# Optimization experiments

Measured on AMD Instinct MI355X. Metric: run time of the kernel, lower is better.

The kernel has to match this reference:

```python
import jax, jax.numpy as jnp
import numpy as np


def setup_inputs() -> dict:
    key = jax.random.key(0)
    k1, k2 = jax.random.split(key)
    B, S, D = 32, 1024, 384
    MAX_MEL_LEN = 8192  # >= max possible sum of durations (7*1024)
    x = jax.random.normal(k1, (B, S, D), dtype=jnp.float32)
    duration = jax.random.randint(k2, (B, S), 0, 8, dtype=jnp.int32)
    return {"x": x, "duration": duration, "max_mel_len": MAX_MEL_LEN}


def reference(x, duration, max_mel_len):
    # x: (B, S, D) float, duration: (B, S) int, max_mel_len: python int
    B, S, D = x.shape
    csum = jnp.cumsum(duration, axis=1)          # (B, S) inclusive cumsum
    mel_len = csum[:, -1]                        # (B,) expanded length per sample
    t = jnp.arange(max_mel_len, dtype=csum.dtype)  # (T,) output frame indices
    # frame t maps to token i where csum[i-1] <= t < csum[i]; side='right'
    # correctly skips zero-duration tokens (repeated csum values)
    idx = jax.vmap(lambda c: jnp.searchsorted(c, t, side='right'))(csum)  # (B, T)
    idx = jnp.clip(idx, 0, S - 1)
    out = jnp.take_along_axis(x, idx[:, :, None], axis=1)  # (B, T, D) gather
    mask = t[None, :] < mel_len[:, None]                   # (B, T) pad mask
    out = out * mask[:, :, None].astype(x.dtype)
    return out, mel_len.astype(jnp.int64)
```

## Files before the change

kernel.cpp:

```cpp
#include <hip/hip_runtime.h>


#define BATCH 32
#define SRC_S 1024
#define DIM   384
#define ROWS  32
#define C4    (DIM / 4)

__global__ void lr_cumsum_kernel(const int* __restrict__ duration,
                                 int* __restrict__ csum,
                                 float* __restrict__ mel_out) {
    __shared__ int s[SRC_S];
    const int b = blockIdx.x;
    const int tid = threadIdx.x;
    s[tid] = duration[b * SRC_S + tid];
    for (int off = 1; off < SRC_S; off <<= 1) {
        __syncthreads();
        const int add = (tid >= off) ? s[tid - off] : 0;
        __syncthreads();
        s[tid] += add;
    }
    __syncthreads();
    csum[b * SRC_S + tid] = s[tid];
    if (tid == SRC_S - 1) {
        mel_out[b] = (float)s[SRC_S - 1];
    }
}

__global__ void lr_gather_kernel(const float* __restrict__ x,
                                 const int* __restrict__ csum,
                                 float* __restrict__ out, int T) {
    __shared__ int c[SRC_S];
    __shared__ int src[ROWS];
    const int b = blockIdx.y;
    const int t0 = blockIdx.x * ROWS;
    const int tid = threadIdx.x;

    ((int4*)c)[tid] = ((const int4*)(csum + b * SRC_S))[tid];
    __syncthreads();

    const int mel_len = c[SRC_S - 1];
    if (tid < ROWS) {
        const int t = t0 + tid;
        int lo = 0, hi = SRC_S;
        while (lo < hi) {
            const int mid = (lo + hi) >> 1;
            if (c[mid] <= t) lo = mid + 1; else hi = mid;
        }
        const int idx = (lo < SRC_S - 1) ? lo : (SRC_S - 1);
        src[tid] = (t < mel_len && t < T) ? idx : ((t < T) ? -1 : -2);
    }
    __syncthreads();

    float4* __restrict__ out4 = (float4*)(out + ((size_t)b * T + t0) * DIM);
    const float4* __restrict__ x4 = (const float4*)(x + (size_t)b * SRC_S * DIM);

    #pragma unroll
    for (int i = tid; i < ROWS * C4; i += 256) {
        const int row = i / C4;
        const int col = i - row * C4;
        const int sidx = src[row];
        if (sidx == -2) continue;
        float4 v = make_float4(0.f, 0.f, 0.f, 0.f);
        if (sidx >= 0) v = x4[(size_t)sidx * C4 + col];
        out4[(size_t)row * C4 + col] = v;
    }
}

extern "C" void kernel_launch(void* const* d_in, const int* in_sizes, int n_in,
                              void* d_out, int out_size, void* d_ws, size_t ws_size,
                              hipStream_t stream) {
    const float* x = (const float*)d_in[0];
    const int* duration = (const int*)d_in[1];
    const int T = (out_size - BATCH) / (BATCH * DIM);

    int* csum = (int*)d_ws;
    float* out = (float*)d_out;
    float* mel_out = out + (size_t)BATCH * T * DIM;

    lr_cumsum_kernel<<<BATCH, SRC_S, 0, stream>>>(duration, csum, mel_out);

    dim3 grid((T + ROWS - 1) / ROWS, BATCH);
    lr_gather_kernel<<<grid, 256, 0, stream>>>(x, csum, out, T);
}
```

Measured before the change: 453.2 us.

## Precompute per-frame source index in scan kernel, drop binary search in gather

The scan kernel now scatters each token's index directly into a per-frame index array (and -1 for padded frames), replacing the csum output. The gather kernel no longer loads csum into shared memory or binary-searches; it reads the precomputed index per row, uses a fixed-trip unrolled loop, and writes output with nontemporal stores. This removes per-block shared loads, syncs and search, at the cost of a larger workspace write in the scan kernel and dropping the tail guard (assumes T divisible by ROWS).

```diff
diff --git a/kernel.cpp b/kernel.cpp
--- a/kernel.cpp
+++ b/kernel.cpp
@@ -7,13 +7,16 @@
 #define ROWS  32
 #define C4    (DIM / 4)
 
-__global__ void lr_cumsum_kernel(const int* __restrict__ duration,
-                                 int* __restrict__ csum,
-                                 float* __restrict__ mel_out) {
+typedef float f32x4 __attribute__((ext_vector_type(4)));
+
+__global__ void lr_scan_idx_kernel(const int* __restrict__ duration,
+                                   int* __restrict__ idx_g,
+                                   float* __restrict__ mel_out, int T) {
     __shared__ int s[SRC_S];
     const int b = blockIdx.x;
     const int tid = threadIdx.x;
-    s[tid] = duration[b * SRC_S + tid];
+    const int d = duration[b * SRC_S + tid];
+    s[tid] = d;
     for (int off = 1; off < SRC_S; off <<= 1) {
         __syncthreads();
         const int add = (tid >= off) ? s[tid - off] : 0;
@@ -21,49 +24,38 @@
         s[tid] += add;
     }
     __syncthreads();
-    csum[b * SRC_S + tid] = s[tid];
-    if (tid == SRC_S - 1) {
-        mel_out[b] = (float)s[SRC_S - 1];
-    }
+    const int end = s[tid];
+    const int start = end - d;
+    const int mel_len = s[SRC_S - 1];
+
+    int* __restrict__ ib = idx_g + (size_t)b * T;
+    for (int t = start; t < end; ++t) ib[t] = tid;
+    for (int t = mel_len + tid; t < T; t += SRC_S) ib[t] = -1;
+
+    if (tid == SRC_S - 1) mel_out[b] = (float)mel_len;
 }
 
-__global__ void lr_gather_kernel(const float* __restrict__ x,
-                                 const int* __restrict__ csum,
-                                 float* __restrict__ out, int T) {
-    __shared__ int c[SRC_S];
-    __shared__ int src[ROWS];
+__global__ __launch_bounds__(256)
+void lr_gather_kernel(const f32x4* __restrict__ x4,
+                      const int* __restrict__ idx_g,
+                      f32x4* __restrict__ out4, int T) {
     const int b = blockIdx.y;
     const int t0 = blockIdx.x * ROWS;
     const int tid = threadIdx.x;
 
-    ((int4*)c)[tid] = ((const int4*)(csum + b * SRC_S))[tid];
-    __syncthreads();
-
-    const int mel_len = c[SRC_S - 1];
-    if (tid < ROWS) {
-        const int t = t0 + tid;
-        int lo = 0, hi = SRC_S;
-        while (lo < hi) {
-            const int mid = (lo + hi) >> 1;
-            if (c[mid] <= t) lo = mid + 1; else hi = mid;
-        }
-        const int idx = (lo < SRC_S - 1) ? lo : (SRC_S - 1);
-        src[tid] = (t < mel_len && t < T) ? idx : ((t < T) ? -1 : -2);
-    }
-    __syncthreads();
-
-    float4* __restrict__ out4 = (float4*)(out + ((size_t)b * T + t0) * DIM);
-    const float4* __restrict__ x4 = (const float4*)(x + (size_t)b * SRC_S * DIM);
+    const int* __restrict__ ib = idx_g + (size_t)b * T + t0;
+    const f32x4* __restrict__ xb = x4 + (size_t)b * SRC_S * C4;
+    f32x4* __restrict__ ob = out4 + ((size_t)b * T + t0) * C4;
 
     #pragma unroll
-    for (int i = tid; i < ROWS * C4; i += 256) {
+    for (int k = 0; k < (ROWS * C4) / 256; ++k) {
+        const int i = tid + k * 256;
         const int row = i / C4;
         const int col = i - row * C4;
-        const int sidx = src[row];
-        if (sidx == -2) continue;
-        float4 v = make_float4(0.f, 0.f, 0.f, 0.f);
-        if (sidx >= 0) v = x4[(size_t)sidx * C4 + col];
-        out4[(size_t)row * C4 + col] = v;
+        const int sidx = ib[row];
+        f32x4 v = (f32x4)(0.f);
+        if (sidx >= 0) v = xb[(size_t)sidx * C4 + col];
+        __builtin_nontemporal_store(v, &ob[i]);
     }
 }
 
@@ -74,12 +66,13 @@
     const int* duration = (const int*)d_in[1];
     const int T = (out_size - BATCH) / (BATCH * DIM);
 
-    int* csum = (int*)d_ws;
+    int* idx_g = (int*)d_ws;
     float* out = (float*)d_out;
     float* mel_out = out + (size_t)BATCH * T * DIM;
 
-    lr_cumsum_kernel<<<BATCH, SRC_S, 0, stream>>>(duration, csum, mel_out);
+    lr_scan_idx_kernel<<<BATCH, SRC_S, 0, stream>>>(duration, idx_g, mel_out, T);
 
     dim3 grid((T + ROWS - 1) / ROWS, BATCH);
-    lr_gather_kernel<<<grid, 256, 0, stream>>>(x, csum, out, T);
+    lr_gather_kernel<<<grid, 256, 0, stream>>>((const f32x4*)x, idx_g,
+                                               (f32x4*)out, T);
 }
```

After: 446.3 us. No clear change (-1.5%).
